# Kernel tuning notes

Measured on AMD Instinct MI355X. Metric: run time of the kernel, lower is better.

## Reference

```python
import jax, jax.numpy as jnp
import numpy as np

GROUP = 8          # weight_group_size
QMAX = 7.0         # 2**(4-1)-1, narrow-range symmetric int4
EPS = 1e-8


def quant_dequant(w):
    """Per-group (size 8, along in_features) symmetric int4 quant-dequant.
    w: [out, in] -> dequantized [out, in]."""
    O, I = w.shape
    wg = w.reshape(O, I // GROUP, GROUP)
    scale = jnp.max(jnp.abs(wg), axis=-1, keepdims=True) / QMAX  # [O, I/G, 1]
    scale = jnp.maximum(scale, EPS)
    q = jnp.clip(jnp.round(wg / scale), -QMAX, QMAX)
    return (q * scale).reshape(O, I)


def setup_inputs() -> dict:
    key = jax.random.key(0)
    kx, kw, kb = jax.random.split(key, 3)
    tokens, din, dout = 8192, 4096, 4096
    x = jax.random.normal(kx, (tokens, din), dtype=jnp.float32)
    weight = jax.random.normal(kw, (dout, din), dtype=jnp.float32) * 0.02
    bias = jax.random.normal(kb, (dout,), dtype=jnp.float32) * 0.01
    return {"x": x, "weight": weight, "bias": bias}


def reference(x, weight, bias):
    w_deq = quant_dequant(weight)                 # [out, in]
    return jnp.dot(x, w_deq.T) + bias             # [tokens, out]
```

## Files before the change

### kernel.cpp

```cpp
#include <hip/hip_runtime.h>
#include <hip/hip_bf16.h>
#include <stdint.h>

typedef __attribute__((ext_vector_type(8))) __bf16 bf16x8;
typedef __attribute__((ext_vector_type(4))) float f32x4;
typedef __attribute__((ext_vector_type(8))) unsigned short ushort8;

typedef const void __attribute__((address_space(1))) gv_t;
typedef void __attribute__((address_space(3))) lv_t;

#define GL16(g, l) __builtin_amdgcn_global_load_lds((gv_t*)(g), (lv_t*)(l), 16, 0, 0)

__device__ __forceinline__ unsigned short f2bf(float f) {
    unsigned int u = __float_as_uint(f);
    u += 0x7fffu + ((u >> 16) & 1u);
    return (unsigned short)(u >> 16);
}

__global__ void __launch_bounds__(256) qdq_weight(const float* __restrict__ w,
                                                  unsigned short* __restrict__ wb,
                                                  int n_groups) {
    int g = blockIdx.x * 256 + threadIdx.x;
    if (g >= n_groups) return;
    const float4* p = (const float4*)w + (size_t)g * 2;
    float4 v0 = p[0], v1 = p[1];
    float t[8] = {v0.x, v0.y, v0.z, v0.w, v1.x, v1.y, v1.z, v1.w};
    float amax = 0.0f;
#pragma unroll
    for (int j = 0; j < 8; ++j) amax = fmaxf(amax, fabsf(t[j]));
    float scale = fmaxf(amax / 7.0f, 1e-8f);
    ushort8 o;
#pragma unroll
    for (int j = 0; j < 8; ++j) {
        float q = rintf(t[j] / scale);
        q = fminf(fmaxf(q, -7.0f), 7.0f);
        o[j] = f2bf(q * scale);
    }
    *((ushort8*)wb + g) = o;
}

__global__ void __launch_bounds__(256) cvt_bf16(const float* __restrict__ x,
                                                unsigned short* __restrict__ xb,
                                                int n8) {
    int i = blockIdx.x * 256 + threadIdx.x;
    if (i >= n8) return;
    const float4* p = (const float4*)x + (size_t)i * 2;
    float4 v0 = p[0], v1 = p[1];
    ushort8 o;
    o[0] = f2bf(v0.x); o[1] = f2bf(v0.y); o[2] = f2bf(v0.z); o[3] = f2bf(v0.w);
    o[4] = f2bf(v1.x); o[5] = f2bf(v1.y); o[6] = f2bf(v1.z); o[7] = f2bf(v1.w);
    *((ushort8*)xb + i) = o;
}

#define BM 256
#define BN 256
#define BK 64

#define MFMA_Q(qm, qn, AF, BF)                                                 \
    __builtin_amdgcn_s_setprio(1);                                             \
    _Pragma("unroll")                                                          \
    for (int mi = 0; mi < 4; ++mi)                                             \
        _Pragma("unroll")                                                      \
        for (int ni = 0; ni < 2; ++ni)                                         \
            _Pragma("unroll")                                                  \
            for (int ks = 0; ks < 2; ++ks)                                     \
                acc[(qm) * 4 + mi][(qn) * 2 + ni] =                            \
                    __builtin_amdgcn_mfma_f32_16x16x32_bf16(                   \
                        AF[mi][ks], BF[ni][ks],                                \
                        acc[(qm) * 4 + mi][(qn) * 2 + ni], 0, 0, 0);           \
    __builtin_amdgcn_s_setprio(0);

#define STAGE_A(b, h, kk)                                                      \
    {                                                                          \
        GL16(gA + (size_t)((h) * 64 + srow) * K + (kk) + schunk,               \
             &sA[b][h][0] + sldso);                                            \
        GL16(gA + (size_t)((h) * 64 + 128 + srow) * K + (kk) + schunk,         \
             &sA[b][h][64 * BK] + sldso);                                      \
    }
#define STAGE_B(b, h, kk)                                                      \
    {                                                                          \
        GL16(gB + (size_t)((h) * 32 + brow) * K + (kk) + schunk,               \
             &sB[b][h][0] + sldso);                                            \
        GL16(gB + (size_t)((h) * 32 + 128 + brow) * K + (kk) + schunk,         \
             &sB[b][h][64 * BK] + sldso);                                      \
    }

#define READ_A(dst, b, h)                                                      \
    _Pragma("unroll")                                                          \
    for (int mi = 0; mi < 4; ++mi) {                                           \
        const int s_ = (wr * 64 + mi * 16 + lr) * BK;                          \
        dst[mi][0] = *(const bf16x8*)&sA[b][h][s_ + e0];                       \
        dst[mi][1] = *(const bf16x8*)&sA[b][h][s_ + e1];                       \
    }
#define READ_B(dst, b, h)                                                      \
    _Pragma("unroll")                                                          \
    for (int ni = 0; ni < 2; ++ni) {                                           \
        const int s_ = (bcol + ni * 16 + lr) * BK;                             \
        dst[ni][0] = *(const bf16x8*)&sB[b][h][s_ + e0];                       \
        dst[ni][1] = *(const bf16x8*)&sB[b][h][s_ + e1];                       \
    }

#define BAR_()     asm volatile("s_barrier" ::: "memory")
#define VM_(n)     asm volatile("s_waitcnt vmcnt(" #n ")" ::: "memory")
#define LGKM_(n)   asm volatile("s_waitcnt lgkmcnt(" #n ")" ::: "memory")
#define SCHEDBAR() __builtin_amdgcn_sched_barrier(0)

#define PHASE(RDS, STG, QM, QN, AF, BF, HINT, VMQ)                             \
    {                                                                          \
        RDS;                                                                   \
        STG;                                                                   \
        HINT;                                                                  \
        BAR_();                                                                \
        LGKM_(0);                                                              \
        SCHEDBAR();                                                            \
        MFMA_Q(QM, QN, AF, BF);                                                \
        VMQ;                                                                   \
        BAR_();                                                                \
    }

__global__ void __launch_bounds__(512, 2)
gemm256(const unsigned short* __restrict__ A,
        const unsigned short* __restrict__ B,
        const float* __restrict__ bias,
        float* __restrict__ C,
        int M, int N, int K) {
    __shared__ unsigned short sA[2][2][128 * BK];
    __shared__ unsigned short sB[2][2][128 * BK];

    const int t  = threadIdx.x;
    const int w  = t >> 6;
    const int ln = t & 63;
    const int lr = ln & 15;
    const int lk = ln >> 4;
    const int wr = w >> 2;
    const int wc = w & 3;
    const int bcol = (wc >> 1) * 64 + (wc & 1) * 32;

    const int nbn = N / BN;
    const int bid = blockIdx.x;
    const int swz = ((int)gridDim.x & 7) ? bid
                  : ((bid & 7) * ((int)gridDim.x >> 3) + (bid >> 3));
    const int m0 = (swz / nbn) * BM;
    const int n0 = (swz % nbn) * BN;

    const unsigned short* gA = A + (size_t)m0 * K;
    const unsigned short* gB = B + (size_t)n0 * K;

    const int srow   = t >> 3;
    const int brow   = (srow & 31) + ((srow >> 5) << 6);
    const int schunk = (((t & 7) ^ (srow & 7)) << 3);
    const int sldso  = (w * 8) * BK;

    const int sw = (lr & 7) << 3;
    const int e0 = (lk * 8) ^ sw;
    const int e1 = (32 + lk * 8) ^ sw;

    f32x4 acc[8][4];
#pragma unroll
    for (int i = 0; i < 8; ++i)
#pragma unroll
        for (int j = 0; j < 4; ++j)
            acc[i][j] = (f32x4)(0.0f);

    const int NT = K / BK;
    const int J  = NT / 2;

    bf16x8 a0f[4][2], a1f[4][2], b0f[2][2], b1f[2][2];

    STAGE_A(0, 0, 0);
    STAGE_B(0, 0, 0);
    STAGE_A(0, 1, 0);
    STAGE_B(0, 1, 0);
    STAGE_A(1, 0, BK);
    STAGE_B(1, 0, BK);
    VM_(4);
    BAR_();

    for (int it = 0; it < J; ++it) {
        const int t0 = 2 * it;
        const int k1 = (t0 + 1) * BK;
        int k2 = (t0 + 2) * BK;  if (k2 >= K) k2 = 0;
        int k3 = (t0 + 3) * BK;  if (k3 >= K) k3 = 0;

        PHASE(READ_A(a0f, 0, 0); READ_B(b0f, 0, 0),
              STAGE_A(1, 1, k1), 0, 0, a0f, b0f, LGKM_(8), );
        PHASE(READ_A(a1f, 0, 1),
              STAGE_B(1, 1, k1), 1, 0, a1f, b0f, , );
        PHASE(READ_B(b1f, 0, 1),
              STAGE_A(0, 0, k2), 1, 1, a1f, b1f, , );
        PHASE(, STAGE_B(0, 0, k2), 0, 1, a0f, b1f, , VM_(4));

        PHASE(READ_A(a0f, 1, 0); READ_B(b0f, 1, 0),
              STAGE_A(0, 1, k2), 0, 0, a0f, b0f, LGKM_(8), );
        PHASE(READ_A(a1f, 1, 1),
              STAGE_B(0, 1, k2), 1, 0, a1f, b0f, , );
        PHASE(READ_B(b1f, 1, 1),
              STAGE_A(1, 0, k3), 1, 1, a1f, b1f, , );
        PHASE(, STAGE_B(1, 0, k3), 0, 1, a0f, b1f, , VM_(4));
    }
    VM_(0);

#pragma unroll
    for (int j = 0; j < 4; ++j) {
        const int n = n0 + wc * 64 + (j >> 1) * 32 + (j & 1) * 16 + lr;
        const float bv = bias[n];
#pragma unroll
        for (int i = 0; i < 8; ++i) {
            const int m = m0 + wr * 128 + (i >> 2) * 64 + (i & 3) * 16 + lk * 4;
            f32x4 v = acc[i][j];
            C[(size_t)(m + 0) * N + n] = v[0] + bv;
            C[(size_t)(m + 1) * N + n] = v[1] + bv;
            C[(size_t)(m + 2) * N + n] = v[2] + bv;
            C[(size_t)(m + 3) * N + n] = v[3] + bv;
        }
    }
}

extern "C" void kernel_launch(void* const* d_in, const int* in_sizes, int n_in,
                              void* d_out, int out_size, void* d_ws, size_t ws_size,
                              hipStream_t stream) {
    const float* x    = (const float*)d_in[0];
    const float* wgt  = (const float*)d_in[1];
    const float* bias = (const float*)d_in[2];
    float* out        = (float*)d_out;

    const int dout = in_sizes[2];
    const int din  = in_sizes[1] / dout;
    const int M    = in_sizes[0] / din;
    const int N    = dout, K = din;

    unsigned short* xb = (unsigned short*)d_ws;
    unsigned short* wb = xb + (size_t)M * K;

    const int ng_w = (N * K) / 8;
    qdq_weight<<<(ng_w + 255) / 256, 256, 0, stream>>>(wgt, wb, ng_w);

    const int n8_x = (M * K) / 8;
    cvt_bf16<<<(n8_x + 255) / 256, 256, 0, stream>>>(x, xb, n8_x);

    const int nwg = (M / BM) * (N / BN);
    gemm256<<<nwg, 512, 0, stream>>>(xb, wb, bias, out, M, N, K);
}
```

Measured before the change: 297.7 us.

## Rebalance GEMM phase schedule to spread LDS reads evenly and deepen prefetch

Restructures the 8-phase main loop so each phase issues exactly one LDS fragment read and one global->LDS stage, with the first fragments read in a prologue. The whole double buffer is filled before the loop and prefetch runs one more tile ahead (kT4), with vmcnt waits at 6 instead of 4. The aim is to even out per-phase LDS traffic and hide global latency better. Buffer-reuse ordering is subtle, so a stage overwriting a half still being read would be a correctness risk.

```diff
diff --git a/kernel.cpp b/kernel.cpp
--- a/kernel.cpp
+++ b/kernel.cpp
@@ -105,11 +105,10 @@
 #define LGKM_(n)   asm volatile("s_waitcnt lgkmcnt(" #n ")" ::: "memory")
 #define SCHEDBAR() __builtin_amdgcn_sched_barrier(0)
 
-#define PHASE(RDS, STG, QM, QN, AF, BF, HINT, VMQ)                             \
+#define PHASE(RDS, STG, QM, QN, AF, BF, VMQ)                                   \
     {                                                                          \
         RDS;                                                                   \
         STG;                                                                   \
-        HINT;                                                                  \
         BAR_();                                                                \
         LGKM_(0);                                                              \
         SCHEDBAR();                                                            \
@@ -167,36 +166,32 @@
 
     bf16x8 a0f[4][2], a1f[4][2], b0f[2][2], b1f[2][2];
 
-    STAGE_A(0, 0, 0);
-    STAGE_B(0, 0, 0);
-    STAGE_A(0, 1, 0);
-    STAGE_B(0, 1, 0);
-    STAGE_A(1, 0, BK);
-    STAGE_B(1, 0, BK);
-    VM_(4);
+    STAGE_A(0, 0, 0);  STAGE_B(0, 0, 0);
+    STAGE_B(0, 1, 0);  STAGE_A(0, 1, 0);
+    STAGE_A(1, 0, BK); STAGE_B(1, 0, BK);
+    STAGE_B(1, 1, BK); STAGE_A(1, 1, BK);
+    VM_(0);
     BAR_();
+    READ_A(a0f, 0, 0);
+    READ_B(b0f, 0, 0);
+    LGKM_(0);
+    BAR_();
+    STAGE_A(0, 0, 2 * BK);
 
     for (int it = 0; it < J; ++it) {
-        const int t0 = 2 * it;
-        const int k1 = (t0 + 1) * BK;
-        int k2 = (t0 + 2) * BK;  if (k2 >= K) k2 = 0;
-        int k3 = (t0 + 3) * BK;  if (k3 >= K) k3 = 0;
-
-        PHASE(READ_A(a0f, 0, 0); READ_B(b0f, 0, 0),
-              STAGE_A(1, 1, k1), 0, 0, a0f, b0f, LGKM_(8), );
-        PHASE(READ_A(a1f, 0, 1),
-              STAGE_B(1, 1, k1), 1, 0, a1f, b0f, , );
-        PHASE(READ_B(b1f, 0, 1),
-              STAGE_A(0, 0, k2), 1, 1, a1f, b1f, , );
-        PHASE(, STAGE_B(0, 0, k2), 0, 1, a0f, b1f, , VM_(4));
-
-        PHASE(READ_A(a0f, 1, 0); READ_B(b0f, 1, 0),
-              STAGE_A(0, 1, k2), 0, 0, a0f, b0f, LGKM_(8), );
-        PHASE(READ_A(a1f, 1, 1),
-              STAGE_B(0, 1, k2), 1, 0, a1f, b0f, , );
-        PHASE(READ_B(b1f, 1, 1),
-              STAGE_A(1, 0, k3), 1, 1, a1f, b1f, , );
-        PHASE(, STAGE_B(1, 0, k3), 0, 1, a0f, b1f, , VM_(4));
+        const int T = 2 * it;
+        int kT2 = (T + 2) * BK;  if (kT2 >= K) kT2 = 0;
+        int kT3 = (T + 3) * BK;  if (kT3 >= K) kT3 = 0;
+        int kT4 = (T + 4) * BK;  if (kT4 >= K) kT4 = 0;
+
+        PHASE(READ_B(b1f, 0, 1), STAGE_B(0, 0, kT2), 0, 0, a0f, b0f, );
+        PHASE(READ_A(a1f, 0, 1), STAGE_B(0, 1, kT2), 0, 1, a0f, b1f, );
+        PHASE(READ_A(a0f, 1, 0), STAGE_A(0, 1, kT2), 1, 0, a1f, b0f, );
+        PHASE(READ_B(b0f, 1, 0), STAGE_A(1, 0, kT3), 1, 1, a1f, b1f, VM_(6));
+        PHASE(READ_B(b1f, 1, 1), STAGE_B(1, 0, kT3), 0, 0, a0f, b0f, );
+        PHASE(READ_A(a1f, 1, 1), STAGE_B(1, 1, kT3), 0, 1, a0f, b1f, );
+        PHASE(READ_A(a0f, 0, 0), STAGE_A(1, 1, kT3), 1, 0, a1f, b0f, );
+        PHASE(READ_B(b0f, 0, 0), STAGE_A(0, 0, kT4), 1, 1, a1f, b1f, VM_(6));
     }
     VM_(0);
 
```

Result: no change. 296.0 us (-0.6%).
